# Performance work log

Measured on AMD Instinct MI355X. Metric: run time of the kernel, lower is better.

Reference implementation:

```python
import jax, jax.numpy as jnp
import numpy as np

N = 50000        # graph_size / n_nodes
E = 1250000      # n_edges
NFEAT = 128
NHID = 64
NCLASS = 47
NLAYERS = 4
DT = 1.0
ALPHA = 1.0


def setup_inputs() -> dict:
    key = jax.random.key(0)
    ks = jax.random.split(key, 12)
    stdv = 1.0 / np.sqrt(NHID)  # reset_params uses uniform(-1/sqrt(nhid), 1/sqrt(nhid))
    u = lambda k, shp: jax.random.uniform(k, shp, jnp.float32, -stdv, stdv)
    return {
        "x": jax.random.normal(ks[0], (N, NFEAT), jnp.float32),
        "edge_index": jax.random.randint(ks[1], (2, E), 0, N, jnp.int32),
        # Linear weights stored as (in, out); torch computes x @ W.T + b, same math.
        "enc_w": u(ks[2], (NFEAT, NHID)),
        "enc_b": u(ks[3], (NHID,)),
        "conv_w": u(ks[4], (NHID, NHID)),   # GCNConv.lin weight (no bias)
        "conv_b": u(ks[5], (NHID,)),        # GCNConv bias (added after aggregation)
        "res_w": u(ks[6], (NHID, NHID)),
        "res_b": u(ks[7], (NHID,)),
        "dec_w": u(ks[8], (NHID, NCLASS)),
        "dec_b": u(ks[9], (NCLASS,)),
        # original inits epsilons to zeros; small noise makes the gate nontrivial
        "epsilons": 0.01 * jax.random.normal(ks[10], (NLAYERS, NHID), jnp.float32),
    }


def reference(x, edge_index, enc_w, enc_b, conv_w, conv_b, res_w, res_b,
              dec_w, dec_b, epsilons):
    n = x.shape[0]
    loop = jnp.arange(n, dtype=edge_index.dtype)
    row = jnp.concatenate([edge_index[0], loop])  # add self-loops (PyG default)
    col = jnp.concatenate([edge_index[1], loop])
    deg = jax.ops.segment_sum(jnp.ones_like(row, x.dtype), col, num_segments=n)
    dinv = jnp.where(deg > 0, jax.lax.rsqrt(deg), 0.0)
    norm = dinv[row] * dinv[col]  # D^{-1/2} (A+I) D^{-1/2}

    # eval mode: dropout is identity
    X = jax.nn.relu(x @ enc_w + enc_b)
    X0 = X
    for i in range(NLAYERS):
        h = X @ conv_w  # conv.lin(X), shared by conv and residual v1
        conv_out = jax.ops.segment_sum(h[row] * norm[:, None], col,
                                       num_segments=n) + conv_b
        res = -(h @ res_w + res_b)          # res_connection_v1
        coeff = 1.0 + jnp.tanh(epsilons[i])[None, :]  # (1, nhid) broadcast over nodes
        X0 = X0 * coeff + DT * (jax.nn.relu(conv_out + res) - ALPHA * X)
        X = X0
    return X @ dec_w + dec_b
```

## Files before the change

### kernel.cpp

```cpp
#include <hip/hip_runtime.h>
#include <hip/hip_bf16.h>
#include <math.h>

#define NFEAT 128
#define NHID 64
#define NCLASS 47
#define NLAYERS 4
#define CAP 80
#define NBUCK 128
#define BSHIFT 9
#define BSLICE 512
#define BCAP 16384
#define BK_EPB 4096
#define AFW 72

typedef __attribute__((ext_vector_type(8))) _Float16 half8;
typedef __attribute__((ext_vector_type(4))) float f32x4;


__global__ __launch_bounds__(256) void k_init(int* __restrict__ gcur,
                                              const float* __restrict__ conv_w,
                                              const float* __restrict__ res_w,
                                              const float* __restrict__ conv_b,
                                              const float* __restrict__ res_b,
                                              const float* __restrict__ eps,
                                              const float* __restrict__ dec_w,
                                              _Float16* __restrict__ Whb,
                                              _Float16* __restrict__ W2hb,
                                              _Float16* __restrict__ Dechb,
                                              float* __restrict__ bc,
                                              float* __restrict__ te) {
    int t = blockIdx.x * 256 + threadIdx.x;
    if (t < 512) {
        int jt = t >> 7, kt = (t >> 6) & 1, l = t & 63;
        int j = jt * 16 + (l & 15);
        int kb = kt * 32 + (l >> 4) * 8;
#pragma unroll
        for (int i = 0; i < 8; ++i)
            Whb[t * 8 + i] = (_Float16)conv_w[(kb + i) * 64 + j];
        return;
    }
    t -= 512;
    if (t < 512) {
        int jt = t >> 7, kt = (t >> 6) & 1, l = t & 63;
        int j = jt * 16 + (l & 15);
        int kb = kt * 32 + (l >> 4) * 8;
#pragma unroll
        for (int i = 0; i < 8; ++i) {
            int k = kb + i;
            float acc = 0.0f;
#pragma unroll 8
            for (int o = 0; o < 64; ++o)
                acc = fmaf(conv_w[k * 64 + o], res_w[o * 64 + j], acc);
            W2hb[t * 8 + i] = (_Float16)acc;
        }
        return;
    }
    t -= 512;
    if (t < 512) {
        int jt = t >> 7, kt = (t >> 6) & 1, l = t & 63;
        int j = jt * 16 + (l & 15);
        int kb = kt * 32 + (l >> 4) * 8;
#pragma unroll
        for (int i = 0; i < 8; ++i) {
            int k = kb + i;
            Dechb[t * 8 + i] = (j < NCLASS) ? (_Float16)dec_w[k * NCLASS + j]
                                            : (_Float16)0.0f;
        }
        return;
    }
    t -= 512;
    if (t < NLAYERS * NHID) {
        te[t] = tanhf(eps[t]);
        if (t < NHID) bc[t] = conv_b[t] - res_b[t];
        if (t < NBUCK) gcur[t] = 0;
    }
}


__global__ __launch_bounds__(256) void k_bucket(const int* __restrict__ row,
                                                const int* __restrict__ col,
                                                int* __restrict__ gcur,
                                                unsigned int* __restrict__ buckets,
                                                int e) {
    __shared__ int lc[BK_EPB];
    __shared__ int lr[BK_EPB];
    __shared__ int cnt[NBUCK], basep[NBUCK], cnt2[NBUCK];
    const int tid = threadIdx.x;
    const int start = blockIdx.x * BK_EPB;
    const int m = min(BK_EPB, e - start);
    for (int i = tid; i < NBUCK; i += 256) { cnt[i] = 0; cnt2[i] = 0; }
    __syncthreads();
    for (int i = tid; i < m; i += 256) {
        int c = col[start + i];
        int r = row[start + i];
        lc[i] = c; lr[i] = r;
        atomicAdd(&cnt[c >> BSHIFT], 1);
    }
    __syncthreads();
    for (int i = tid; i < NBUCK; i += 256)
        if (cnt[i] > 0) basep[i] = atomicAdd(&gcur[i], cnt[i]);
    __syncthreads();
    for (int i = tid; i < m; i += 256) {
        int c = lc[i], r = lr[i];
        int s = c >> BSHIFT;
        int dst = basep[s] + atomicAdd(&cnt2[s], 1);
        if (dst < BCAP)
            buckets[(size_t)s * BCAP + dst] = ((unsigned)r << 16) | (unsigned)c;
    }
}


__global__ __launch_bounds__(256) void k_fill2(const unsigned int* __restrict__ buckets,
                                               const int* __restrict__ gcur,
                                               int* __restrict__ deg,
                                               unsigned short* __restrict__ csr,
                                               int n) {
    __shared__ int cur[BSLICE];
    const int s = blockIdx.x;
    const int tid = threadIdx.x;
    for (int i = tid; i < BSLICE; i += 256) cur[i] = 0;
    __syncthreads();
    const int cnt = min(gcur[s], BCAP);
    const unsigned int* bp = buckets + (size_t)s * BCAP;
    for (int i = tid; i < cnt; i += 256) {
        unsigned int v = bp[i];
        int c = (int)(v & 0xffffu);
        int r = (int)(v >> 16);
        int pos = atomicAdd(&cur[c & (BSLICE - 1)], 1);
        if (pos < CAP) csr[(size_t)c * CAP + pos] = (unsigned short)r;
    }
    __syncthreads();
    const int base = s * BSLICE;
    const int nb = min(BSLICE, n - base);
    for (int i = tid; i < nb; i += 256) deg[base + i] = cur[i];
}


__global__ void k_dinv(const int* __restrict__ deg, float* __restrict__ dinv,
                       float* __restrict__ rsq, unsigned short* __restrict__ csr,
                       _Float16* __restrict__ Y0, _Float16* __restrict__ Y1, int n) {
    int i = blockIdx.x * blockDim.x + threadIdx.x;
    if (i < n) {
        int d = deg[i];
        if (d > CAP) d = CAP;
        float d1 = (float)(deg[i] + 1);
        dinv[i] = rsqrtf(d1);
        rsq[i] = sqrtf(d1);
        int end = (d + 7) & ~7;
        if (end > CAP) end = CAP;
        for (int s = d; s < end; ++s)
            csr[(size_t)i * CAP + s] = (unsigned short)n;
    }
    if (i < NHID) {
        Y0[(size_t)n * NHID + i] = (_Float16)0.0f;
        Y1[(size_t)n * NHID + i] = (_Float16)0.0f;
    }
}


__global__ __launch_bounds__(256) void k_encoder(const float* __restrict__ x,
                                                 const float* __restrict__ w,
                                                 const float* __restrict__ b,
                                                 const float* __restrict__ dinv,
                                                 _Float16* __restrict__ Y, int n) {
    __shared__ float xs[16][NFEAT];
    const int wid = threadIdx.x >> 6;
    const int j = threadIdx.x & 63;
    const int base = blockIdx.x * 16 + wid * 4;
    for (int m = 0; m < 4; ++m) {
        int node = base + m;
        float a = 0.f, c = 0.f;
        if (node < n) {
            a = x[node * NFEAT + j];
            c = x[node * NFEAT + 64 + j];
        }
        xs[wid * 4 + m][j] = a;
        xs[wid * 4 + m][j + 64] = c;
    }
    float acc[4] = {0.f, 0.f, 0.f, 0.f};
#pragma unroll 4
    for (int k4 = 0; k4 < NFEAT / 4; ++k4) {
        int k = k4 * 4;
        float w0 = w[(k + 0) * 64 + j];
        float w1 = w[(k + 1) * 64 + j];
        float w2 = w[(k + 2) * 64 + j];
        float w3 = w[(k + 3) * 64 + j];
        for (int m = 0; m < 4; ++m) {
            const float4 xv = *reinterpret_cast<const float4*>(&xs[wid * 4 + m][k]);
            acc[m] = fmaf(xv.x, w0, fmaf(xv.y, w1, fmaf(xv.z, w2, fmaf(xv.w, w3, acc[m]))));
        }
    }
    float bj = b[j];
    for (int m = 0; m < 4; ++m) {
        int node = base + m;
        if (node < n) {
            float v = fmaxf(acc[m] + bj, 0.0f);
            Y[node * NHID + j] = (_Float16)(v * dinv[node]);
        }
    }
}


__global__ __launch_bounds__(256, 4) void k_layer(
    const half8* __restrict__ Y8c, _Float16* __restrict__ Ynext,
    const int* __restrict__ deg, const unsigned short* __restrict__ csr,
    const float* __restrict__ dinv, const float* __restrict__ rsq,
    const half8* __restrict__ Whb, const half8* __restrict__ W2hb,
    const half8* __restrict__ Dechb,
    const float* __restrict__ bc, const float* __restrict__ te,
    const float* __restrict__ dec_b, float* __restrict__ out, int n, int last) {
    __shared__ _Float16 Af[16][AFW];
    __shared__ _Float16 Xf[16][AFW];
    const int wid = threadIdx.x >> 6;
    const int lane = threadIdx.x & 63;
    const int g = lane >> 4;
    const int l = lane & 15;
    const int c = l & 7;
    const unsigned sh = (l & 8) << 1;
    const int base = blockIdx.x * 16 + wid * 4;
    const int mynode = base + g;
    const bool gact = mynode < n;
    const int gn = gact ? mynode : 0;
    const int rown = gact ? mynode : n;
    const float dcg = dinv[gn];
    const float rcg = rsq[gn];
    int d = gact ? deg[gn] : 0;
    if (d > CAP) d = CAP;
    const int nit = (d + 7) >> 3;

    float acc[8] = {0.f, 0.f, 0.f, 0.f, 0.f, 0.f, 0.f, 0.f};
    const uint4* cp = reinterpret_cast<const uint4*>(csr + (size_t)gn * CAP);

    uint4 rA = cp[0];
    int a0 = (int)((rA.x >> sh) & 0xffffu);
    int a1 = (int)((rA.y >> sh) & 0xffffu);
    int a2 = (int)((rA.z >> sh) & 0xffffu);
    int a3 = (int)((rA.w >> sh) & 0xffffu);
    half8 A0 = Y8c[(size_t)(a0 * 8 + c)];
    half8 A1 = Y8c[(size_t)(a1 * 8 + c)];
    half8 A2 = Y8c[(size_t)(a2 * 8 + c)];
    half8 A3 = Y8c[(size_t)(a3 * 8 + c)];
    int it = 0;
    for (; it + 1 < nit; it += 2) {
        uint4 rB = cp[it + 1];
        int b0 = (int)((rB.x >> sh) & 0xffffu);
        int b1 = (int)((rB.y >> sh) & 0xffffu);
        int b2 = (int)((rB.z >> sh) & 0xffffu);
        int b3 = (int)((rB.w >> sh) & 0xffffu);
        half8 B0 = Y8c[(size_t)(b0 * 8 + c)];
        half8 B1 = Y8c[(size_t)(b1 * 8 + c)];
        half8 B2 = Y8c[(size_t)(b2 * 8 + c)];
        half8 B3 = Y8c[(size_t)(b3 * 8 + c)];
#pragma unroll
        for (int i = 0; i < 8; ++i)
            acc[i] += ((float)A0[i] + (float)A1[i]) + ((float)A2[i] + (float)A3[i]);
        rA = cp[it + 2];
        a0 = (int)((rA.x >> sh) & 0xffffu);
        a1 = (int)((rA.y >> sh) & 0xffffu);
        a2 = (int)((rA.z >> sh) & 0xffffu);
        a3 = (int)((rA.w >> sh) & 0xffffu);
        A0 = Y8c[(size_t)(a0 * 8 + c)];
        A1 = Y8c[(size_t)(a1 * 8 + c)];
        A2 = Y8c[(size_t)(a2 * 8 + c)];
        A3 = Y8c[(size_t)(a3 * 8 + c)];
#pragma unroll
        for (int i = 0; i < 8; ++i)
            acc[i] += ((float)B0[i] + (float)B1[i]) + ((float)B2[i] + (float)B3[i]);
    }
    if (it < nit) {
#pragma unroll
        for (int i = 0; i < 8; ++i)
            acc[i] += ((float)A0[i] + (float)A1[i]) + ((float)A2[i] + (float)A3[i]);
    }
#pragma unroll
    for (int i = 0; i < 8; ++i) acc[i] += __shfl_xor(acc[i], 8);

    if (l < 8) {
        half8 yc = Y8c[(size_t)(rown * 8 + c)];
        half8 hg, hx;
#pragma unroll
        for (int i = 0; i < 8; ++i) {
            float ycf = (float)yc[i];
            hg[i] = (_Float16)((acc[i] + ycf) * dcg);
            hx[i] = (_Float16)(ycf * rcg);
        }
        *reinterpret_cast<half8*>(&Af[wid * 4 + g][c * 8]) = hg;
        *reinterpret_cast<half8*>(&Xf[wid * 4 + g][c * 8]) = hx;
    }

    float dv[4];
#pragma unroll
    for (int i = 0; i < 4; ++i) dv[i] = __shfl(dcg, i * 16);

    const int ar = (wid * 4 + (lane & 15)) & 15;
    const int aq = (lane >> 4) * 8;
    half8 aG0 = *reinterpret_cast<const half8*>(&Af[ar][aq]);
    half8 aG1 = *reinterpret_cast<const half8*>(&Af[ar][32 + aq]);
    half8 aX0 = *reinterpret_cast<const half8*>(&Xf[ar][aq]);
    half8 aX1 = *reinterpret_cast<const half8*>(&Xf[ar][32 + aq]);
    const f32x4 zero = {0.f, 0.f, 0.f, 0.f};

#pragma unroll
    for (int jt = 0; jt < 4; ++jt) {
        half8 bG0 = Whb[(jt * 2 + 0) * 64 + lane];
        half8 bG1 = Whb[(jt * 2 + 1) * 64 + lane];
        half8 bX0 = W2hb[(jt * 2 + 0) * 64 + lane];
        half8 bX1 = W2hb[(jt * 2 + 1) * 64 + lane];
        f32x4 dG = __builtin_amdgcn_mfma_f32_16x16x32_f16(aG0, bG0, zero, 0, 0, 0);
        dG = __builtin_amdgcn_mfma_f32_16x16x32_f16(aG1, bG1, dG, 0, 0, 0);
        f32x4 dX = __builtin_amdgcn_mfma_f32_16x16x32_f16(aX0, bX0, zero, 0, 0, 0);
        dX = __builtin_amdgcn_mfma_f32_16x16x32_f16(aX1, bX1, dX, 0, 0, 0);
        if (lane < 16) {
            int j = jt * 16 + lane;
            float tej = te[j], bcj = bc[j];
#pragma unroll
            for (int i = 0; i < 4; ++i) {
                int node = base + i;
                float xf = (float)Xf[wid * 4 + i][j];
                float xn = xf * tej + fmaxf(dG[i] + bcj - dX[i], 0.0f);
                if (!last) {
                    if (node < n)
                        Ynext[(size_t)node * NHID + j] = (_Float16)(xn * dv[i]);
                } else {
                    Af[wid * 4 + i][j] = (_Float16)xn;
                }
            }
        }
    }

    if (last) {
        half8 aD0 = *reinterpret_cast<const half8*>(&Af[ar][aq]);
        half8 aD1 = *reinterpret_cast<const half8*>(&Af[ar][32 + aq]);
#pragma unroll
        for (int jt = 0; jt < 4; ++jt) {
            half8 bD0 = Dechb[(jt * 2 + 0) * 64 + lane];
            half8 bD1 = Dechb[(jt * 2 + 1) * 64 + lane];
            f32x4 dd = __builtin_amdgcn_mfma_f32_16x16x32_f16(aD0, bD0, zero, 0, 0, 0);
            dd = __builtin_amdgcn_mfma_f32_16x16x32_f16(aD1, bD1, dd, 0, 0, 0);
            if (lane < 16) {
                int j = jt * 16 + lane;
                if (j < NCLASS) {
                    float db = dec_b[j];
#pragma unroll
                    for (int i = 0; i < 4; ++i) {
                        int node = base + i;
                        if (node < n) out[(size_t)node * NCLASS + j] = dd[i] + db;
                    }
                }
            }
        }
    }
}

extern "C" void kernel_launch(void* const* d_in, const int* in_sizes, int n_in,
                              void* d_out, int out_size, void* d_ws, size_t ws_size,
                              hipStream_t stream) {
    const float* x      = (const float*)d_in[0];
    const int*   edges  = (const int*)d_in[1];
    const float* enc_w  = (const float*)d_in[2];
    const float* enc_b  = (const float*)d_in[3];
    const float* conv_w = (const float*)d_in[4];
    const float* conv_b = (const float*)d_in[5];
    const float* res_w  = (const float*)d_in[6];
    const float* res_b  = (const float*)d_in[7];
    const float* dec_w  = (const float*)d_in[8];
    const float* dec_b  = (const float*)d_in[9];
    const float* eps    = (const float*)d_in[10];
    float* out = (float*)d_out;

    const int n = in_sizes[0] / NFEAT;
    const int e = in_sizes[1] / 2;
    const int* row = edges;
    const int* col = edges + e;

    char* p = (char*)d_ws;
    unsigned short* csr = (unsigned short*)p;
    p += ((size_t)n * CAP * 2 + 64 + 15) & ~(size_t)15;
    unsigned int* buckets = (unsigned int*)p;  p += (size_t)NBUCK * BCAP * 4;
    _Float16* Y0 = (_Float16*)p;  p += (((size_t)(n + 1) * NHID * 2 + 15) & ~(size_t)15);
    _Float16* Y1 = (_Float16*)p;  p += (((size_t)(n + 1) * NHID * 2 + 15) & ~(size_t)15);
    int*   deg  = (int*)p;    p += (size_t)n * 4;
    float* dinv = (float*)p;  p += (size_t)n * 4;
    float* rsq  = (float*)p;  p += (size_t)n * 4;
    int*   gcur = (int*)p;    p += ((NBUCK + 15) & ~15) * 4;
    float* bc   = (float*)p;  p += NHID * 4;
    float* te   = (float*)p;  p += NLAYERS * NHID * 4;
    _Float16* Whb   = (_Float16*)p;  p += 4096 * 2;
    _Float16* W2hb  = (_Float16*)p;  p += 4096 * 2;
    _Float16* Dechb = (_Float16*)p;  p += 4096 * 2;
    if ((size_t)(p - (char*)d_ws) > ws_size) return;

    k_init<<<7, 256, 0, stream>>>(gcur, conv_w, res_w, conv_b, res_b,
                                  eps, dec_w, Whb, W2hb, Dechb, bc, te);
    const int bblocks = (e + BK_EPB - 1) / BK_EPB;
    k_bucket<<<bblocks, 256, 0, stream>>>(row, col, gcur, buckets, e);
    k_fill2<<<NBUCK, 256, 0, stream>>>(buckets, gcur, deg, csr, n);
    k_dinv<<<(n + 255) / 256, 256, 0, stream>>>(deg, dinv, rsq, csr, Y0, Y1, n);

    const int tblocks = (n + 15) / 16;
    k_encoder<<<tblocks, 256, 0, stream>>>(x, enc_w, enc_b, dinv, Y0, n);

    for (int l = 0; l < NLAYERS; ++l) {
        _Float16* ycur = (l & 1) ? Y1 : Y0;
        _Float16* ynxt = (l & 1) ? Y0 : Y1;
        k_layer<<<tblocks, 256, 0, stream>>>((const half8*)ycur, ynxt, deg, csr,
                                             dinv, rsq, (const half8*)Whb,
                                             (const half8*)W2hb, (const half8*)Dechb,
                                             bc, te + l * NHID, dec_b, out, n,
                                             (l == NLAYERS - 1) ? 1 : 0);
    }
}
```

Before: 229.8 us.

## Use MFMA for encoder, deepen gather prefetch, halve bucket block size

The encoder matmul moves from scalar fp32 FMAs to fp16 MFMA 16x16x32 instructions. The encoder weights are pre-packed to fp16 in k_init, and x is staged in LDS as fp16. The layer gather loop gets a three-stage rolling prefetch instead of two-stage unrolling, so more neighbour loads are in flight. Edges per bucket block drop from 4096 to 2048, giving more blocks. Converting x to fp16 costs some precision, and the deeper prefetch raises register pressure.

```diff
diff --git a/kernel.cpp b/kernel.cpp
--- a/kernel.cpp
+++ b/kernel.cpp
@@ -11,26 +11,39 @@
 #define BSHIFT 9
 #define BSLICE 512
 #define BCAP 16384
-#define BK_EPB 4096
+#define BK_EPB 2048
 #define AFW 72
+#define XEW 136
 
 typedef __attribute__((ext_vector_type(8))) _Float16 half8;
 typedef __attribute__((ext_vector_type(4))) float f32x4;
 
 
 __global__ __launch_bounds__(256) void k_init(int* __restrict__ gcur,
+                                              const float* __restrict__ enc_w,
                                               const float* __restrict__ conv_w,
                                               const float* __restrict__ res_w,
                                               const float* __restrict__ conv_b,
                                               const float* __restrict__ res_b,
                                               const float* __restrict__ eps,
                                               const float* __restrict__ dec_w,
+                                              _Float16* __restrict__ Enchb,
                                               _Float16* __restrict__ Whb,
                                               _Float16* __restrict__ W2hb,
                                               _Float16* __restrict__ Dechb,
                                               float* __restrict__ bc,
                                               float* __restrict__ te) {
     int t = blockIdx.x * 256 + threadIdx.x;
+    if (t < 1024) {
+        int jt = t >> 8, kt = (t >> 6) & 3, l = t & 63;
+        int j = jt * 16 + (l & 15);
+        int kb = kt * 32 + (l >> 4) * 8;
+#pragma unroll
+        for (int i = 0; i < 8; ++i)
+            Enchb[t * 8 + i] = (_Float16)enc_w[(kb + i) * 64 + j];
+        return;
+    }
+    t -= 1024;
     if (t < 512) {
         int jt = t >> 7, kt = (t >> 6) & 1, l = t & 63;
         int j = jt * 16 + (l & 15);
@@ -160,43 +173,59 @@
 
 
 __global__ __launch_bounds__(256) void k_encoder(const float* __restrict__ x,
-                                                 const float* __restrict__ w,
+                                                 const half8* __restrict__ Enchb,
                                                  const float* __restrict__ b,
                                                  const float* __restrict__ dinv,
                                                  _Float16* __restrict__ Y, int n) {
-    __shared__ float xs[16][NFEAT];
+    __shared__ _Float16 Xe[16][XEW];
     const int wid = threadIdx.x >> 6;
-    const int j = threadIdx.x & 63;
+    const int lane = threadIdx.x & 63;
     const int base = blockIdx.x * 16 + wid * 4;
-    for (int m = 0; m < 4; ++m) {
-        int node = base + m;
-        float a = 0.f, c = 0.f;
+
+    {
+        int nl = wid * 4 + ((threadIdx.x >> 4) & 3);
+        int seg = threadIdx.x & 15;
+        int node = blockIdx.x * 16 + nl;
+        float4 u = make_float4(0.f, 0.f, 0.f, 0.f), v = u;
         if (node < n) {
-            a = x[node * NFEAT + j];
-            c = x[node * NFEAT + 64 + j];
-        }
-        xs[wid * 4 + m][j] = a;
-        xs[wid * 4 + m][j + 64] = c;
-    }
-    float acc[4] = {0.f, 0.f, 0.f, 0.f};
-#pragma unroll 4
-    for (int k4 = 0; k4 < NFEAT / 4; ++k4) {
-        int k = k4 * 4;
-        float w0 = w[(k + 0) * 64 + j];
-        float w1 = w[(k + 1) * 64 + j];
-        float w2 = w[(k + 2) * 64 + j];
-        float w3 = w[(k + 3) * 64 + j];
-        for (int m = 0; m < 4; ++m) {
-            const float4 xv = *reinterpret_cast<const float4*>(&xs[wid * 4 + m][k]);
-            acc[m] = fmaf(xv.x, w0, fmaf(xv.y, w1, fmaf(xv.z, w2, fmaf(xv.w, w3, acc[m]))));
-        }
-    }
-    float bj = b[j];
-    for (int m = 0; m < 4; ++m) {
-        int node = base + m;
-        if (node < n) {
-            float v = fmaxf(acc[m] + bj, 0.0f);
-            Y[node * NHID + j] = (_Float16)(v * dinv[node]);
+            const float4* xp = reinterpret_cast<const float4*>(x + (size_t)node * NFEAT + seg * 8);
+            u = xp[0]; v = xp[1];
+        }
+        half8 h;
+        h[0] = (_Float16)u.x; h[1] = (_Float16)u.y; h[2] = (_Float16)u.z; h[3] = (_Float16)u.w;
+        h[4] = (_Float16)v.x; h[5] = (_Float16)v.y; h[6] = (_Float16)v.z; h[7] = (_Float16)v.w;
+        *reinterpret_cast<half8*>(&Xe[nl][seg * 8]) = h;
+    }
+
+    const int ar = (wid * 4 + (lane & 15)) & 15;
+    const int aq = (lane >> 4) * 8;
+    half8 a0 = *reinterpret_cast<const half8*>(&Xe[ar][0 * 32 + aq]);
+    half8 a1 = *reinterpret_cast<const half8*>(&Xe[ar][1 * 32 + aq]);
+    half8 a2 = *reinterpret_cast<const half8*>(&Xe[ar][2 * 32 + aq]);
+    half8 a3 = *reinterpret_cast<const half8*>(&Xe[ar][3 * 32 + aq]);
+    const f32x4 zero = {0.f, 0.f, 0.f, 0.f};
+
+    float dvv[4];
+#pragma unroll
+    for (int i = 0; i < 4; ++i) dvv[i] = (base + i < n) ? dinv[base + i] : 0.f;
+
+#pragma unroll
+    for (int jt = 0; jt < 4; ++jt) {
+        f32x4 dacc = __builtin_amdgcn_mfma_f32_16x16x32_f16(a0, Enchb[(jt * 4 + 0) * 64 + lane], zero, 0, 0, 0);
+        dacc = __builtin_amdgcn_mfma_f32_16x16x32_f16(a1, Enchb[(jt * 4 + 1) * 64 + lane], dacc, 0, 0, 0);
+        dacc = __builtin_amdgcn_mfma_f32_16x16x32_f16(a2, Enchb[(jt * 4 + 2) * 64 + lane], dacc, 0, 0, 0);
+        dacc = __builtin_amdgcn_mfma_f32_16x16x32_f16(a3, Enchb[(jt * 4 + 3) * 64 + lane], dacc, 0, 0, 0);
+        if (lane < 16) {
+            int j = jt * 16 + lane;
+            float bj = b[j];
+#pragma unroll
+            for (int i = 0; i < 4; ++i) {
+                int node = base + i;
+                if (node < n) {
+                    float v = fmaxf(dacc[i] + bj, 0.0f);
+                    Y[(size_t)node * NHID + j] = (_Float16)(v * dvv[i]);
+                }
+            }
         }
     }
 }
@@ -232,46 +261,51 @@
     float acc[8] = {0.f, 0.f, 0.f, 0.f, 0.f, 0.f, 0.f, 0.f};
     const uint4* cp = reinterpret_cast<const uint4*>(csr + (size_t)gn * CAP);
 
-    uint4 rA = cp[0];
-    int a0 = (int)((rA.x >> sh) & 0xffffu);
-    int a1 = (int)((rA.y >> sh) & 0xffffu);
-    int a2 = (int)((rA.z >> sh) & 0xffffu);
-    int a3 = (int)((rA.w >> sh) & 0xffffu);
+    uint4 rt = cp[0];
+    int a0 = (int)((rt.x >> sh) & 0xffffu);
+    int a1 = (int)((rt.y >> sh) & 0xffffu);
+    int a2 = (int)((rt.z >> sh) & 0xffffu);
+    int a3 = (int)((rt.w >> sh) & 0xffffu);
     half8 A0 = Y8c[(size_t)(a0 * 8 + c)];
     half8 A1 = Y8c[(size_t)(a1 * 8 + c)];
     half8 A2 = Y8c[(size_t)(a2 * 8 + c)];
     half8 A3 = Y8c[(size_t)(a3 * 8 + c)];
+    rt = cp[1];
+    int b0 = (int)((rt.x >> sh) & 0xffffu);
+    int b1 = (int)((rt.y >> sh) & 0xffffu);
+    int b2 = (int)((rt.z >> sh) & 0xffffu);
+    int b3 = (int)((rt.w >> sh) & 0xffffu);
+    half8 B0 = Y8c[(size_t)(b0 * 8 + c)];
+    half8 B1 = Y8c[(size_t)(b1 * 8 + c)];
+    half8 B2 = Y8c[(size_t)(b2 * 8 + c)];
+    half8 B3 = Y8c[(size_t)(b3 * 8 + c)];
+    uint4 rc2 = cp[2];
     int it = 0;
-    for (; it + 1 < nit; it += 2) {
-        uint4 rB = cp[it + 1];
-        int b0 = (int)((rB.x >> sh) & 0xffffu);
-        int b1 = (int)((rB.y >> sh) & 0xffffu);
-        int b2 = (int)((rB.z >> sh) & 0xffffu);
-        int b3 = (int)((rB.w >> sh) & 0xffffu);
-        half8 B0 = Y8c[(size_t)(b0 * 8 + c)];
-        half8 B1 = Y8c[(size_t)(b1 * 8 + c)];
-        half8 B2 = Y8c[(size_t)(b2 * 8 + c)];
-        half8 B3 = Y8c[(size_t)(b3 * 8 + c)];
+    for (; it + 2 < nit; ++it) {
+        int c0 = (int)((rc2.x >> sh) & 0xffffu);
+        int c1 = (int)((rc2.y >> sh) & 0xffffu);
+        int c2 = (int)((rc2.z >> sh) & 0xffffu);
+        int c3 = (int)((rc2.w >> sh) & 0xffffu);
+        half8 C0 = Y8c[(size_t)(c0 * 8 + c)];
+        half8 C1 = Y8c[(size_t)(c1 * 8 + c)];
+        half8 C2 = Y8c[(size_t)(c2 * 8 + c)];
+        half8 C3 = Y8c[(size_t)(c3 * 8 + c)];
+        rc2 = cp[it + 3];
 #pragma unroll
         for (int i = 0; i < 8; ++i)
             acc[i] += ((float)A0[i] + (float)A1[i]) + ((float)A2[i] + (float)A3[i]);
-        rA = cp[it + 2];
-        a0 = (int)((rA.x >> sh) & 0xffffu);
-        a1 = (int)((rA.y >> sh) & 0xffffu);
-        a2 = (int)((rA.z >> sh) & 0xffffu);
-        a3 = (int)((rA.w >> sh) & 0xffffu);
-        A0 = Y8c[(size_t)(a0 * 8 + c)];
-        A1 = Y8c[(size_t)(a1 * 8 + c)];
-        A2 = Y8c[(size_t)(a2 * 8 + c)];
-        A3 = Y8c[(size_t)(a3 * 8 + c)];
+        A0 = B0; A1 = B1; A2 = B2; A3 = B3;
+        B0 = C0; B1 = C1; B2 = C2; B3 = C3;
+    }
+    if (it < nit) {
+#pragma unroll
+        for (int i = 0; i < 8; ++i)
+            acc[i] += ((float)A0[i] + (float)A1[i]) + ((float)A2[i] + (float)A3[i]);
+    }
+    if (it + 1 < nit) {
 #pragma unroll
         for (int i = 0; i < 8; ++i)
             acc[i] += ((float)B0[i] + (float)B1[i]) + ((float)B2[i] + (float)B3[i]);
-    }
-    if (it < nit) {
-#pragma unroll
-        for (int i = 0; i < 8; ++i)
-            acc[i] += ((float)A0[i] + (float)A1[i]) + ((float)A2[i] + (float)A3[i]);
     }
 #pragma unroll
     for (int i = 0; i < 8; ++i) acc[i] += __shfl_xor(acc[i], 8);
@@ -386,20 +420,21 @@
     int*   gcur = (int*)p;    p += ((NBUCK + 15) & ~15) * 4;
     float* bc   = (float*)p;  p += NHID * 4;
     float* te   = (float*)p;  p += NLAYERS * NHID * 4;
+    _Float16* Enchb = (_Float16*)p;  p += 8192 * 2;
     _Float16* Whb   = (_Float16*)p;  p += 4096 * 2;
     _Float16* W2hb  = (_Float16*)p;  p += 4096 * 2;
     _Float16* Dechb = (_Float16*)p;  p += 4096 * 2;
     if ((size_t)(p - (char*)d_ws) > ws_size) return;
 
-    k_init<<<7, 256, 0, stream>>>(gcur, conv_w, res_w, conv_b, res_b,
-                                  eps, dec_w, Whb, W2hb, Dechb, bc, te);
+    k_init<<<11, 256, 0, stream>>>(gcur, enc_w, conv_w, res_w, conv_b, res_b,
+                                   eps, dec_w, Enchb, Whb, W2hb, Dechb, bc, te);
     const int bblocks = (e + BK_EPB - 1) / BK_EPB;
     k_bucket<<<bblocks, 256, 0, stream>>>(row, col, gcur, buckets, e);
     k_fill2<<<NBUCK, 256, 0, stream>>>(buckets, gcur, deg, csr, n);
     k_dinv<<<(n + 255) / 256, 256, 0, stream>>>(deg, dinv, rsq, csr, Y0, Y1, n);
 
     const int tblocks = (n + 15) / 16;
-    k_encoder<<<tblocks, 256, 0, stream>>>(x, enc_w, enc_b, dinv, Y0, n);
+    k_encoder<<<tblocks, 256, 0, stream>>>(x, (const half8*)Enchb, enc_b, dinv, Y0, n);
 
     for (int l = 0; l < NLAYERS; ++l) {
         _Float16* ycur = (l & 1) ? Y1 : Y0;
```

Result: faster. 222.9 us (-3.0%).
